# Performance work log

Measured on AMD Instinct MI355X. Metric: run time of the kernel, lower is better.

## Reference

```python
import jax, jax.numpy as jnp
import numpy as np
import math

# Config: 8 packed images, each a 32x32 patch grid (t=1) -> equal seglen 1024
NSEG, GH, GW = 8, 32, 32
L = GH * GW            # 1024 tokens per segment
S = NSEG * L           # 8192 packed tokens
H, NH = 1024, 16
HD = H // NH           # 64, head dim (rope dim), divisible by 4
MLP = 4096
THETA = 10000.0


def _make_rope_cos_sin():
    # Rope2DPosEmb._precompute_freqs_cis for a (GH, GW) grid, dim=HD
    flat = np.arange(L, dtype=np.float32)
    x_pos = flat % GW
    y_pos = flat // GW
    dim_range = np.arange(0, HD, 4, dtype=np.float32)[: HD // 4]
    freqs = 1.0 / THETA ** (dim_range / HD)          # [HD//4]
    x_f = np.outer(x_pos, freqs)                     # [L, HD//4]
    y_f = np.outer(y_pos, freqs)
    # interleave x/y angles per frequency -> [L, HD//2]
    ang = np.stack([x_f, y_f], axis=-1).reshape(L, HD // 2)
    ang = np.tile(ang, (NSEG, 1))                    # same grid repeated per image
    return jnp.asarray(np.cos(ang)), jnp.asarray(np.sin(ang))


def setup_inputs() -> dict:
    key = jax.random.key(0)
    ks = jax.random.split(key, 8)
    cos, sin = _make_rope_cos_sin()
    inp = {
        "x": jax.random.normal(ks[0], (S, H), jnp.float32),
        "wqkv": jax.random.normal(ks[1], (3 * H, H), jnp.float32) * math.sqrt(1.0 / H),
        "wo": jax.random.normal(ks[2], (H, H), jnp.float32) * math.sqrt(1.0 / H),
        "ln0_g": jnp.ones((H,), jnp.float32),
        "ln0_b": jnp.zeros((H,), jnp.float32),
        "ln1_g": jnp.ones((H,), jnp.float32),
        "ln1_b": jnp.zeros((H,), jnp.float32),
        "fc0_w": jax.random.normal(ks[3], (MLP, H), jnp.float32) * math.sqrt(2.0 / H),
        "fc0_b": jnp.zeros((MLP,), jnp.float32),
        "fc1_w": jax.random.normal(ks[4], (H, MLP), jnp.float32) * math.sqrt(2.0 / MLP),
        "fc1_b": jnp.zeros((H,), jnp.float32),
        "rope_cos": cos,
        "rope_sin": sin,
        "cu_seqlens": jnp.arange(NSEG + 1, dtype=jnp.int32) * L,
    }
    return inp


def _layernorm(x, g, b, eps=1e-5):
    m = x.mean(-1, keepdims=True)
    v = ((x - m) ** 2).mean(-1, keepdims=True)
    return (x - m) * jax.lax.rsqrt(v + eps) * g + b


def _apply_rope(x, cos, sin):
    # x: [S, NH, HD]; cos/sin: [S, HD//2]. Complex mult on (even, odd) pairs.
    xr = x.reshape(S, NH, HD // 2, 2)
    x0, x1 = xr[..., 0], xr[..., 1]
    c = cos[:, None, :]
    s = sin[:, None, :]
    o0 = x0 * c - x1 * s
    o1 = x0 * s + x1 * c
    return jnp.stack([o0, o1], axis=-1).reshape(S, NH, HD)


def reference(x, wqkv, wo, ln0_g, ln0_b, ln1_g, ln1_b,
              fc0_w, fc0_b, fc1_w, fc1_b, rope_cos, rope_sin, cu_seqlens):
    # --- attention branch (pre-norm) ---
    h = _layernorm(x, ln0_g, ln0_b)
    qkv = (h @ wqkv.T).reshape(S, 3, NH, HD)
    q, k, v = qkv[:, 0], qkv[:, 1], qkv[:, 2]
    q = _apply_rope(q, rope_cos, rope_sin)
    k = _apply_rope(k, rope_cos, rope_sin)
    # block-diagonal varlen attention: equal-length segments -> reshape
    qb = q.reshape(NSEG, L, NH, HD)
    kb = k.reshape(NSEG, L, NH, HD)
    vb = v.reshape(NSEG, L, NH, HD)
    scores = jnp.einsum("blhd,bmhd->bhlm", qb, kb) / math.sqrt(HD)
    p = jax.nn.softmax(scores.astype(jnp.float32), axis=-1).astype(x.dtype)
    attn = jnp.einsum("bhlm,bmhd->blhd", p, vb).reshape(S, H)
    x = x + attn @ wo.T
    # --- MLP branch (pre-norm) ---
    h2 = _layernorm(x, ln1_g, ln1_b)
    mlp = jax.nn.gelu(h2 @ fc0_w.T + fc0_b, approximate=False) @ fc1_w.T + fc1_b
    return x + mlp
```

## Files before the change

### kernel.cpp

```cpp
#include <hip/hip_runtime.h>
#include <math.h>


typedef __bf16 bf16x8 __attribute__((ext_vector_type(8)));
typedef float f32x4 __attribute__((ext_vector_type(4)));
typedef float f32x16 __attribute__((ext_vector_type(16)));
typedef unsigned int u32;

__device__ __forceinline__ unsigned short f2b(float f) {
  unsigned u = __float_as_uint(f);
  return (unsigned short)((u + 0x7FFFu + ((u >> 16) & 1u)) >> 16);
}
__device__ __forceinline__ float b2f(unsigned short h) {
  return __uint_as_float(((unsigned)h) << 16);
}
__device__ __forceinline__ void async_ld16(const void* g, void* l) {
  __builtin_amdgcn_global_load_lds((__attribute__((address_space(1))) void*)g,
                                   (__attribute__((address_space(3))) void*)l,
                                   16, 0, 0);
}
__device__ __forceinline__ float exp2fast(float x) {
#if __has_builtin(__builtin_amdgcn_exp2f)
  return __builtin_amdgcn_exp2f(x);
#else
  return exp2f(x);
#endif
}
__device__ __forceinline__ float rcpfast(float x) {
#if __has_builtin(__builtin_amdgcn_rcpf)
  return __builtin_amdgcn_rcpf(x);
#else
  return 1.0f / x;
#endif
}

__global__ __launch_bounds__(256) void castall_kernel(
    const float* __restrict__ s0, const float* __restrict__ s1,
    const float* __restrict__ s2, const float* __restrict__ s3,
    unsigned short* __restrict__ dst) {
  const int t = blockIdx.x * 256 + threadIdx.x;
  const float* src;
  int off;
  if (t < 786432) { src = s0; off = t; }
  else if (t < 1048576) { src = s1; off = t - 786432; }
  else if (t < 2097152) { src = s2; off = t - 1048576; }
  else { src = s3; off = t - 2097152; }
  const float4 v = ((const float4*)src)[off];
  ushort4 o;
  o.x = f2b(v.x); o.y = f2b(v.y); o.z = f2b(v.z); o.w = f2b(v.w);
  ((ushort4*)dst)[t] = o;
}

__global__ __launch_bounds__(256) void ln_kernel(const float* __restrict__ x,
                                                 const float* __restrict__ g,
                                                 const float* __restrict__ bt,
                                                 unsigned short* __restrict__ out) {
  __shared__ float red[8];
  const int row = blockIdx.x, t = threadIdx.x;
  const float4 v = ((const float4*)(x + (size_t)row * 1024))[t];
  float s = v.x + v.y + v.z + v.w;
  float s2 = v.x * v.x + v.y * v.y + v.z * v.z + v.w * v.w;
#pragma unroll
  for (int m = 1; m < 64; m <<= 1) {
    s += __shfl_xor(s, m, 64);
    s2 += __shfl_xor(s2, m, 64);
  }
  if ((t & 63) == 0) { red[t >> 6] = s; red[4 + (t >> 6)] = s2; }
  __syncthreads();
  const float ts = red[0] + red[1] + red[2] + red[3];
  const float ts2 = red[4] + red[5] + red[6] + red[7];
  const float mean = ts * (1.f / 1024.f);
  const float var = ts2 * (1.f / 1024.f) - mean * mean;
  const float inv = rsqrtf(var + 1e-5f);
  const float4 gv = ((const float4*)g)[t];
  const float4 bv = ((const float4*)bt)[t];
  ushort4 o;
  o.x = f2b((v.x - mean) * inv * gv.x + bv.x);
  o.y = f2b((v.y - mean) * inv * gv.y + bv.y);
  o.z = f2b((v.z - mean) * inv * gv.z + bv.z);
  o.w = f2b((v.w - mean) * inv * gv.w + bv.w);
  ((ushort4*)out)[(size_t)row * 256 + t] = o;
}

template <int MODE>
__global__ __launch_bounds__(256) void gemm_bt(
    const unsigned short* __restrict__ A, const unsigned short* __restrict__ B,
    int M, int N, int K, float* __restrict__ outf, unsigned short* __restrict__ outb,
    const float* __restrict__ res, const float* __restrict__ bias) {
  __shared__ __align__(16) unsigned short As[128 * 32];
  __shared__ __align__(16) unsigned short Bs[128 * 32];
  const int bm = blockIdx.y * 128, bn = blockIdx.x * 128;
  const int t = threadIdx.x, wave = t >> 6, lane = t & 63;
  const int quad = lane >> 4, l16 = lane & 15;
  const int wm = (wave >> 1) * 64, wn = (wave & 1) * 64;
  const int srow = lane >> 2;
  const int scol = (((lane & 3) ^ ((lane >> 3) & 3)) * 8);
  const unsigned short* Ag0 = A + (size_t)(bm + wave * 32 + srow) * K + scol;
  const unsigned short* Ag1 = Ag0 + (size_t)16 * K;
  const unsigned short* Bg0 = B + (size_t)(bn + wave * 32 + srow) * K + scol;
  const unsigned short* Bg1 = Bg0 + (size_t)16 * K;
  unsigned short* Al = As + wave * 1024;
  unsigned short* Bl = Bs + wave * 1024;
  const int swg = (l16 >> 1) & 3;
  f32x4 acc[4][4] = {};
  for (int k0 = 0; k0 < K; k0 += 32) {
    async_ld16(Ag0 + k0, Al);
    async_ld16(Ag1 + k0, Al + 512);
    async_ld16(Bg0 + k0, Bl);
    async_ld16(Bg1 + k0, Bl + 512);
    __syncthreads();
    bf16x8 af[4], bfv[4];
#pragma unroll
    for (int i = 0; i < 4; i++)
      af[i] = *(const bf16x8*)(As + (wm + i * 16 + l16) * 32 + (quad ^ swg) * 8);
#pragma unroll
    for (int j = 0; j < 4; j++)
      bfv[j] = *(const bf16x8*)(Bs + (wn + j * 16 + l16) * 32 + (quad ^ swg) * 8);
#pragma unroll
    for (int i = 0; i < 4; i++)
#pragma unroll
      for (int j = 0; j < 4; j++)
        acc[i][j] = __builtin_amdgcn_mfma_f32_16x16x32_bf16(af[i], bfv[j], acc[i][j], 0, 0, 0);
    __syncthreads();
  }
#pragma unroll
  for (int i = 0; i < 4; i++)
#pragma unroll
    for (int j = 0; j < 4; j++)
#pragma unroll
      for (int r = 0; r < 4; r++) {
        const int m = bm + wm + i * 16 + quad * 4 + r;
        const int n = bn + wn + j * 16 + l16;
        const size_t idx = (size_t)m * N + n;
        const float v = acc[i][j][r];
        if (MODE == 1) {
          outf[idx] = v + res[idx];
        } else if (MODE == 2) {
          const float z = v + bias[n];
          const float u = z * (0.7978845608f + 0.03567740814f * z * z);
          const float e = fminf(u * 2.885390082f, 80.f);
          const float tt = exp2fast(e);
          outb[idx] = f2b(z * tt * rcpfast(tt + 1.0f));
        } else if (MODE == 3) {
          outf[idx] = v + bias[n] + res[idx];
        } else {
          outb[idx] = f2b(v);
        }
      }
}

__device__ __forceinline__ u32 rope2(u32 in, float c, float sn, float sc) {
  const float a = b2f((unsigned short)(in & 0xffff));
  const float b = b2f((unsigned short)(in >> 16));
  return (u32)f2b((a * c - b * sn) * sc) | ((u32)f2b((a * sn + b * c) * sc) << 16);
}
__global__ __launch_bounds__(256) void rope_kernel(const unsigned short* __restrict__ qkv,
                                                   const float* __restrict__ cb,
                                                   const float* __restrict__ sb,
                                                   unsigned short* __restrict__ qh,
                                                   unsigned short* __restrict__ kh) {
  const int tid = blockIdx.x * 256 + threadIdx.x;
  const int ii = tid & 7, head = (tid >> 3) & 15, s = tid >> 7;
  const float4 cv = *(const float4*)(cb + s * 32 + ii * 4);
  const float4 sv = *(const float4*)(sb + s * 32 + ii * 4);
  const unsigned short* base = qkv + (size_t)s * 3072 + head * 64 + ii * 8;
  const uint4 qa = *(const uint4*)base;
  const uint4 ka = *(const uint4*)(base + 1024);
  const int seg = s >> 10, l = s & 1023;
  const size_t o = ((size_t)((seg * 16 + head) * 1024 + l)) * 64 + ii * 8;
  const float QSC = 0.125f * 1.44269504f;
  uint4 qo, ko;
  qo.x = rope2(qa.x, cv.x, sv.x, QSC); ko.x = rope2(ka.x, cv.x, sv.x, 1.f);
  qo.y = rope2(qa.y, cv.y, sv.y, QSC); ko.y = rope2(ka.y, cv.y, sv.y, 1.f);
  qo.z = rope2(qa.z, cv.z, sv.z, QSC); ko.z = rope2(ka.z, cv.z, sv.z, 1.f);
  qo.w = rope2(qa.w, cv.w, sv.w, QSC); ko.w = rope2(ka.w, cv.w, sv.w, 1.f);
  *(uint4*)(qh + o) = qo;
  *(uint4*)(kh + o) = ko;
}

__global__ __launch_bounds__(256) void vtrans_kernel(const unsigned short* __restrict__ qkv,
                                                     unsigned short* __restrict__ vt) {
  __shared__ unsigned short tile[64][72];
  const int b = blockIdx.x;
  const int lt = b & 15, head = (b >> 4) & 15, seg = b >> 8;
  const int t = threadIdx.x;
  const int r = t >> 2, c0 = (t & 3) * 16;
  const unsigned short* src =
      qkv + ((size_t)(seg * 1024 + lt * 64 + r)) * 3072 + 2048 + head * 64 + c0;
#pragma unroll
  for (int k = 0; k < 16; k++) tile[r][c0 + k] = src[k];
  __syncthreads();
  unsigned short* dst =
      vt + ((size_t)((seg * 16 + head) * 64 + r)) * 1024 + lt * 64 + c0;
#pragma unroll
  for (int k = 0; k < 16; k++) dst[k] = tile[c0 + k][r];
}

__global__ __launch_bounds__(256) void attn_kernel(const unsigned short* __restrict__ qh,
                                                   const unsigned short* __restrict__ kh,
                                                   const unsigned short* __restrict__ vt,
                                                   unsigned short* __restrict__ out) {
  __shared__ __align__(16) unsigned short Qs[128 * 64];
  __shared__ __align__(16) unsigned short Ks[64 * 64];
  __shared__ __align__(16) unsigned short Vs[64 * 64];
  __shared__ float wl[128];
  const int b = blockIdx.x;
  const int head = b & 15, seg = (b >> 4) & 7, qt = b >> 7;
  const int t = threadIdx.x, wave = t >> 6, lane = t & 63;
  const int h = lane >> 5, q31 = lane & 31;
  const size_t sh = (size_t)(seg * 16 + head);
  const unsigned short* qbase = qh + (sh * 1024 + (size_t)qt * 128) * 64;
  const unsigned short* kbase = kh + sh * 1024 * 64;
  const unsigned short* vbase = vt + sh * 64 * 1024;
  const int r8 = lane >> 3;
  const int c8 = ((lane & 7) ^ (r8 & 7)) * 8;
#pragma unroll
  for (int cc = 0; cc < 4; cc++) {
    const int chunk = wave * 4 + cc;
    async_ld16(qbase + (size_t)(chunk * 8 + r8) * 64 + c8, Qs + chunk * 512);
  }
  const int qrow_l = wave * 32 + q31;
  const int qsw = qrow_l & 7;
  bf16x8 qf[4];
  float lsum = 0.f;
  f32x16 oacc[2] = {};

  for (int kt = 0; kt < 16; kt++) {
    const int ch0 = wave * 2;
    async_ld16(kbase + (size_t)(kt * 64 + ch0 * 8 + r8) * 64 + c8, Ks + ch0 * 512);
    async_ld16(kbase + (size_t)(kt * 64 + ch0 * 8 + 8 + r8) * 64 + c8, Ks + ch0 * 512 + 512);
    async_ld16(vbase + (size_t)(ch0 * 8 + r8) * 1024 + kt * 64 + c8, Vs + ch0 * 512);
    async_ld16(vbase + (size_t)(ch0 * 8 + 8 + r8) * 1024 + kt * 64 + c8, Vs + ch0 * 512 + 512);
    __syncthreads();
    if (kt == 0) {
#pragma unroll
      for (int ks = 0; ks < 4; ks++)
        qf[ks] = *(const bf16x8*)(Qs + qrow_l * 64 + (((2 * ks + h) ^ qsw)) * 8);
    }
    f32x16 st[2] = {{}, {}};
#pragma unroll
    for (int T = 0; T < 2; T++) {
      const int krow = 32 * T + q31;
      const int ksw = krow & 7;
#pragma unroll
      for (int ks = 0; ks < 4; ks++) {
        const bf16x8 kf = *(const bf16x8*)(Ks + krow * 64 + (((2 * ks + h) ^ ksw)) * 8);
        st[T] = __builtin_amdgcn_mfma_f32_32x32x16_bf16(kf, qf[ks], st[T], 0, 0, 0);
      }
    }
    u32 pk[2][4][2];
#pragma unroll
    for (int T = 0; T < 2; T++)
#pragma unroll
      for (int g = 0; g < 4; g++)
#pragma unroll
        for (int e = 0; e < 2; e++) {
          const float plo = exp2fast(st[T][4 * g + 2 * e]);
          const float phi = exp2fast(st[T][4 * g + 2 * e + 1]);
          lsum += plo + phi;
          pk[T][g][e] = (u32)f2b(plo) | ((u32)f2b(phi) << 16);
        }
    u32 rcv[2][4];
#pragma unroll
    for (int T = 0; T < 2; T++) {
      const u32 p0 = h ? pk[T][0][0] : pk[T][1][0];
      const u32 p1 = h ? pk[T][0][1] : pk[T][1][1];
      const u32 p2 = h ? pk[T][2][0] : pk[T][3][0];
      const u32 p3 = h ? pk[T][2][1] : pk[T][3][1];
      rcv[T][0] = (u32)__shfl_xor((int)p0, 32, 64);
      rcv[T][1] = (u32)__shfl_xor((int)p1, 32, 64);
      rcv[T][2] = (u32)__shfl_xor((int)p2, 32, 64);
      rcv[T][3] = (u32)__shfl_xor((int)p3, 32, 64);
    }
#pragma unroll
    for (int tt = 0; tt < 4; tt++) {
      const int T = tt >> 1, uu = tt & 1;
      union { u32 u[4]; bf16x8 v; } af;
      if (h == 0) {
        af.u[0] = pk[T][2 * uu][0];
        af.u[1] = pk[T][2 * uu][1];
        af.u[2] = rcv[T][2 * uu];
        af.u[3] = rcv[T][2 * uu + 1];
      } else {
        af.u[0] = rcv[T][2 * uu];
        af.u[1] = rcv[T][2 * uu + 1];
        af.u[2] = pk[T][2 * uu + 1][0];
        af.u[3] = pk[T][2 * uu + 1][1];
      }
#pragma unroll
      for (int ot = 0; ot < 2; ot++) {
        const int vrow = 32 * ot + q31;
        const int vsw = vrow & 7;
        const bf16x8 bv = *(const bf16x8*)(Vs + vrow * 64 + (((2 * tt + h) ^ vsw)) * 8);
        oacc[ot] = __builtin_amdgcn_mfma_f32_32x32x16_bf16(af.v, bv, oacc[ot], 0, 0, 0);
      }
    }
    __syncthreads();
  }
  lsum += __shfl_xor(lsum, 32, 64);
  if (h == 0) wl[wave * 32 + q31] = lsum;
  const int qglob = seg * 1024 + qt * 128 + wave * 32;
#pragma unroll
  for (int g = 0; g < 4; g++) {
    const float4 lv = *(const float4*)&wl[wave * 32 + 8 * g + 4 * h];
#pragma unroll
    for (int m = 0; m < 4; m++) {
      const int r16 = 4 * g + m;
      const int qrow = qglob + m + 8 * g + 4 * h;
      const float invl = rcpfast((&lv.x)[m]);
#pragma unroll
      for (int ot = 0; ot < 2; ot++)
        out[(size_t)qrow * 1024 + head * 64 + 32 * ot + q31] = f2b(oacc[ot][r16] * invl);
    }
  }
}

extern "C" void kernel_launch(void* const* d_in, const int* in_sizes, int n_in,
                              void* d_out, int out_size, void* d_ws, size_t ws_size,
                              hipStream_t stream) {
  (void)in_sizes; (void)n_in; (void)out_size; (void)ws_size;
  const float* x    = (const float*)d_in[0];
  const float* wqkv = (const float*)d_in[1];
  const float* wo   = (const float*)d_in[2];
  const float* ln0g = (const float*)d_in[3];
  const float* ln0b = (const float*)d_in[4];
  const float* ln1g = (const float*)d_in[5];
  const float* ln1b = (const float*)d_in[6];
  const float* fc0w = (const float*)d_in[7];
  const float* fc0b = (const float*)d_in[8];
  const float* fc1w = (const float*)d_in[9];
  const float* fc1b = (const float*)d_in[10];
  const float* rc   = (const float*)d_in[11];
  const float* rsn  = (const float*)d_in[12];
  float* out = (float*)d_out;
  char* w = (char*)d_ws;
  const size_t MB = 1u << 20;
  unsigned short* hb    = (unsigned short*)(w + 0);
  unsigned short* bqkv  = (unsigned short*)(w + 16 * MB);
  unsigned short* bwo   = (unsigned short*)(w + 22 * MB);
  unsigned short* bfc0  = (unsigned short*)(w + 24 * MB);
  unsigned short* bfc1  = (unsigned short*)(w + 32 * MB);
  unsigned short* qhb   = (unsigned short*)(w + 40 * MB);
  unsigned short* khb   = (unsigned short*)(w + 56 * MB);
  unsigned short* vtb   = (unsigned short*)(w + 72 * MB);
  unsigned short* attnb = (unsigned short*)(w + 88 * MB);
  unsigned short* qkvb  = (unsigned short*)(w + 104 * MB);
  unsigned short* midb  = (unsigned short*)(w + 104 * MB);

  castall_kernel<<<12288, 256, 0, stream>>>(wqkv, wo, fc0w, fc1w, bqkv);
  ln_kernel<<<8192, 256, 0, stream>>>(x, ln0g, ln0b, hb);
  gemm_bt<4><<<dim3(24, 64), 256, 0, stream>>>(hb, bqkv, 8192, 3072, 1024,
                                               nullptr, qkvb, nullptr, nullptr);
  rope_kernel<<<4096, 256, 0, stream>>>(qkvb, rc, rsn, qhb, khb);
  vtrans_kernel<<<2048, 256, 0, stream>>>(qkvb, vtb);
  attn_kernel<<<1024, 256, 0, stream>>>(qhb, khb, vtb, attnb);
  gemm_bt<1><<<dim3(8, 64), 256, 0, stream>>>(attnb, bwo, 8192, 1024, 1024,
                                              out, nullptr, x, nullptr);
  ln_kernel<<<8192, 256, 0, stream>>>(out, ln1g, ln1b, hb);
  gemm_bt<2><<<dim3(32, 64), 256, 0, stream>>>(hb, bfc0, 8192, 4096, 1024,
                                               nullptr, midb, nullptr, fc0b);
  gemm_bt<3><<<dim3(8, 64), 256, 0, stream>>>(midb, bfc1, 8192, 1024, 4096,
                                              out, nullptr, out, fc1b);
}
```

Measured before the change: 545.7 us.

## Fuse cast with layernorm, fuse rope with V transpose, split-K the FC1 GEMM

```diff
diff --git a/kernel.cpp b/kernel.cpp
--- a/kernel.cpp
+++ b/kernel.cpp
@@ -34,21 +34,52 @@
 #endif
 }
 
-__global__ __launch_bounds__(256) void castall_kernel(
-    const float* __restrict__ s0, const float* __restrict__ s1,
-    const float* __restrict__ s2, const float* __restrict__ s3,
-    unsigned short* __restrict__ dst) {
-  const int t = blockIdx.x * 256 + threadIdx.x;
-  const float* src;
-  int off;
-  if (t < 786432) { src = s0; off = t; }
-  else if (t < 1048576) { src = s1; off = t - 786432; }
-  else if (t < 2097152) { src = s2; off = t - 1048576; }
-  else { src = s3; off = t - 2097152; }
-  const float4 v = ((const float4*)src)[off];
+__global__ __launch_bounds__(256) void castln_kernel(
+    const float* __restrict__ w0, const float* __restrict__ w1,
+    const float* __restrict__ w2, const float* __restrict__ w3,
+    unsigned short* __restrict__ wdst,
+    const float* __restrict__ x, const float* __restrict__ g,
+    const float* __restrict__ bt, unsigned short* __restrict__ hout) {
+  __shared__ float red[8];
+  const int blk = blockIdx.x;
+  if (blk < 12288) {
+    const int t = blk * 256 + threadIdx.x;
+    const float* src;
+    int off;
+    if (t < 786432) { src = w0; off = t; }
+    else if (t < 1048576) { src = w1; off = t - 786432; }
+    else if (t < 2097152) { src = w2; off = t - 1048576; }
+    else { src = w3; off = t - 2097152; }
+    const float4 v = ((const float4*)src)[off];
+    ushort4 o;
+    o.x = f2b(v.x); o.y = f2b(v.y); o.z = f2b(v.z); o.w = f2b(v.w);
+    ((ushort4*)wdst)[t] = o;
+    return;
+  }
+  const int row = blk - 12288, t = threadIdx.x;
+  const float4 v = ((const float4*)(x + (size_t)row * 1024))[t];
+  float s = v.x + v.y + v.z + v.w;
+  float s2 = v.x * v.x + v.y * v.y + v.z * v.z + v.w * v.w;
+#pragma unroll
+  for (int m = 1; m < 64; m <<= 1) {
+    s += __shfl_xor(s, m, 64);
+    s2 += __shfl_xor(s2, m, 64);
+  }
+  if ((t & 63) == 0) { red[t >> 6] = s; red[4 + (t >> 6)] = s2; }
+  __syncthreads();
+  const float ts = red[0] + red[1] + red[2] + red[3];
+  const float ts2 = red[4] + red[5] + red[6] + red[7];
+  const float mean = ts * (1.f / 1024.f);
+  const float var = ts2 * (1.f / 1024.f) - mean * mean;
+  const float inv = rsqrtf(var + 1e-5f);
+  const float4 gv = ((const float4*)g)[t];
+  const float4 bv = ((const float4*)bt)[t];
   ushort4 o;
-  o.x = f2b(v.x); o.y = f2b(v.y); o.z = f2b(v.z); o.w = f2b(v.w);
-  ((ushort4*)dst)[t] = o;
+  o.x = f2b((v.x - mean) * inv * gv.x + bv.x);
+  o.y = f2b((v.y - mean) * inv * gv.y + bv.y);
+  o.z = f2b((v.z - mean) * inv * gv.z + bv.z);
+  o.w = f2b((v.w - mean) * inv * gv.w + bv.w);
+  ((ushort4*)hout)[(size_t)row * 256 + t] = o;
 }
 
 __global__ __launch_bounds__(256) void ln_kernel(const float* __restrict__ x,
@@ -86,10 +117,13 @@
 __global__ __launch_bounds__(256) void gemm_bt(
     const unsigned short* __restrict__ A, const unsigned short* __restrict__ B,
     int M, int N, int K, float* __restrict__ outf, unsigned short* __restrict__ outb,
-    const float* __restrict__ res, const float* __restrict__ bias) {
+    const float* __restrict__ res, const float* __restrict__ bias,
+    float* __restrict__ part) {
   __shared__ __align__(16) unsigned short As[128 * 32];
   __shared__ __align__(16) unsigned short Bs[128 * 32];
   const int bm = blockIdx.y * 128, bn = blockIdx.x * 128;
+  const int Kper = K / gridDim.z;
+  const int kbeg = blockIdx.z * Kper, kend = kbeg + Kper;
   const int t = threadIdx.x, wave = t >> 6, lane = t & 63;
   const int quad = lane >> 4, l16 = lane & 15;
   const int wm = (wave >> 1) * 64, wn = (wave & 1) * 64;
@@ -103,7 +137,7 @@
   unsigned short* Bl = Bs + wave * 1024;
   const int swg = (l16 >> 1) & 3;
   f32x4 acc[4][4] = {};
-  for (int k0 = 0; k0 < K; k0 += 32) {
+  for (int k0 = kbeg; k0 < kend; k0 += 32) {
     async_ld16(Ag0 + k0, Al);
     async_ld16(Ag1 + k0, Al + 512);
     async_ld16(Bg0 + k0, Bl);
@@ -141,12 +175,22 @@
           const float e = fminf(u * 2.885390082f, 80.f);
           const float tt = exp2fast(e);
           outb[idx] = f2b(z * tt * rcpfast(tt + 1.0f));
-        } else if (MODE == 3) {
-          outf[idx] = v + bias[n] + res[idx];
+        } else if (MODE == 4) {
+          outb[idx] = f2b(v);
         } else {
-          outb[idx] = f2b(v);
+          if (blockIdx.z == 0) outf[idx] = v + bias[n] + res[idx];
+          else part[idx] = v;
         }
       }
+}
+
+__global__ __launch_bounds__(256) void addp_kernel(float* __restrict__ out,
+                                                   const float* __restrict__ p) {
+  const int t = blockIdx.x * 256 + threadIdx.x;
+  float4 a = ((const float4*)out)[t];
+  const float4 b = ((const float4*)p)[t];
+  a.x += b.x; a.y += b.y; a.z += b.z; a.w += b.w;
+  ((float4*)out)[t] = a;
 }
 
 __device__ __forceinline__ u32 rope2(u32 in, float c, float sn, float sc) {
@@ -154,34 +198,35 @@
   const float b = b2f((unsigned short)(in >> 16));
   return (u32)f2b((a * c - b * sn) * sc) | ((u32)f2b((a * sn + b * c) * sc) << 16);
 }
-__global__ __launch_bounds__(256) void rope_kernel(const unsigned short* __restrict__ qkv,
-                                                   const float* __restrict__ cb,
-                                                   const float* __restrict__ sb,
-                                                   unsigned short* __restrict__ qh,
-                                                   unsigned short* __restrict__ kh) {
-  const int tid = blockIdx.x * 256 + threadIdx.x;
-  const int ii = tid & 7, head = (tid >> 3) & 15, s = tid >> 7;
-  const float4 cv = *(const float4*)(cb + s * 32 + ii * 4);
-  const float4 sv = *(const float4*)(sb + s * 32 + ii * 4);
-  const unsigned short* base = qkv + (size_t)s * 3072 + head * 64 + ii * 8;
-  const uint4 qa = *(const uint4*)base;
-  const uint4 ka = *(const uint4*)(base + 1024);
-  const int seg = s >> 10, l = s & 1023;
-  const size_t o = ((size_t)((seg * 16 + head) * 1024 + l)) * 64 + ii * 8;
-  const float QSC = 0.125f * 1.44269504f;
-  uint4 qo, ko;
-  qo.x = rope2(qa.x, cv.x, sv.x, QSC); ko.x = rope2(ka.x, cv.x, sv.x, 1.f);
-  qo.y = rope2(qa.y, cv.y, sv.y, QSC); ko.y = rope2(ka.y, cv.y, sv.y, 1.f);
-  qo.z = rope2(qa.z, cv.z, sv.z, QSC); ko.z = rope2(ka.z, cv.z, sv.z, 1.f);
-  qo.w = rope2(qa.w, cv.w, sv.w, QSC); ko.w = rope2(ka.w, cv.w, sv.w, 1.f);
-  *(uint4*)(qh + o) = qo;
-  *(uint4*)(kh + o) = ko;
-}
-
-__global__ __launch_bounds__(256) void vtrans_kernel(const unsigned short* __restrict__ qkv,
+__global__ __launch_bounds__(256) void ropevt_kernel(const unsigned short* __restrict__ qkv,
+                                                     const float* __restrict__ cb,
+                                                     const float* __restrict__ sb,
+                                                     unsigned short* __restrict__ qh,
+                                                     unsigned short* __restrict__ kh,
                                                      unsigned short* __restrict__ vt) {
   __shared__ unsigned short tile[64][72];
-  const int b = blockIdx.x;
+  const int blk = blockIdx.x;
+  if (blk < 4096) {
+    const int tid = blk * 256 + threadIdx.x;
+    const int ii = tid & 7, head = (tid >> 3) & 15, s = tid >> 7;
+    const float4 cv = *(const float4*)(cb + s * 32 + ii * 4);
+    const float4 sv = *(const float4*)(sb + s * 32 + ii * 4);
+    const unsigned short* base = qkv + (size_t)s * 3072 + head * 64 + ii * 8;
+    const uint4 qa = *(const uint4*)base;
+    const uint4 ka = *(const uint4*)(base + 1024);
+    const int seg = s >> 10, l = s & 1023;
+    const size_t o = ((size_t)((seg * 16 + head) * 1024 + l)) * 64 + ii * 8;
+    const float QSC = 0.125f * 1.44269504f;
+    uint4 qo, ko;
+    qo.x = rope2(qa.x, cv.x, sv.x, QSC); ko.x = rope2(ka.x, cv.x, sv.x, 1.f);
+    qo.y = rope2(qa.y, cv.y, sv.y, QSC); ko.y = rope2(ka.y, cv.y, sv.y, 1.f);
+    qo.z = rope2(qa.z, cv.z, sv.z, QSC); ko.z = rope2(ka.z, cv.z, sv.z, 1.f);
+    qo.w = rope2(qa.w, cv.w, sv.w, QSC); ko.w = rope2(ka.w, cv.w, sv.w, 1.f);
+    *(uint4*)(qh + o) = qo;
+    *(uint4*)(kh + o) = ko;
+    return;
+  }
+  const int b = blk - 4096;
   const int lt = b & 15, head = (b >> 4) & 15, seg = b >> 8;
   const int t = threadIdx.x;
   const int r = t >> 2, c0 = (t & 3) * 16;
@@ -346,19 +391,20 @@
   unsigned short* attnb = (unsigned short*)(w + 88 * MB);
   unsigned short* qkvb  = (unsigned short*)(w + 104 * MB);
   unsigned short* midb  = (unsigned short*)(w + 104 * MB);
-
-  castall_kernel<<<12288, 256, 0, stream>>>(wqkv, wo, fc0w, fc1w, bqkv);
-  ln_kernel<<<8192, 256, 0, stream>>>(x, ln0g, ln0b, hb);
+  float* p1 = (float*)(w + 40 * MB);
+
+  castln_kernel<<<20480, 256, 0, stream>>>(wqkv, wo, fc0w, fc1w, bqkv,
+                                           x, ln0g, ln0b, hb);
   gemm_bt<4><<<dim3(24, 64), 256, 0, stream>>>(hb, bqkv, 8192, 3072, 1024,
-                                               nullptr, qkvb, nullptr, nullptr);
-  rope_kernel<<<4096, 256, 0, stream>>>(qkvb, rc, rsn, qhb, khb);
-  vtrans_kernel<<<2048, 256, 0, stream>>>(qkvb, vtb);
+                                               nullptr, qkvb, nullptr, nullptr, nullptr);
+  ropevt_kernel<<<6144, 256, 0, stream>>>(qkvb, rc, rsn, qhb, khb, vtb);
   attn_kernel<<<1024, 256, 0, stream>>>(qhb, khb, vtb, attnb);
   gemm_bt<1><<<dim3(8, 64), 256, 0, stream>>>(attnb, bwo, 8192, 1024, 1024,
-                                              out, nullptr, x, nullptr);
+                                              out, nullptr, x, nullptr, nullptr);
   ln_kernel<<<8192, 256, 0, stream>>>(out, ln1g, ln1b, hb);
   gemm_bt<2><<<dim3(32, 64), 256, 0, stream>>>(hb, bfc0, 8192, 4096, 1024,
-                                               nullptr, midb, nullptr, fc0b);
-  gemm_bt<3><<<dim3(8, 64), 256, 0, stream>>>(midb, bfc1, 8192, 1024, 4096,
-                                              out, nullptr, out, fc1b);
-}
+                                               nullptr, midb, nullptr, fc0b, nullptr);
+  gemm_bt<6><<<dim3(8, 64, 2), 256, 0, stream>>>(midb, bfc1, 8192, 1024, 4096,
+                                                 out, nullptr, out, fc1b, p1);
+  addp_kernel<<<8192, 256, 0, stream>>>(out, p1);
+}
```

New measurement: 586.9 us. +7.6%, slower.
